# Kernel tuning notes

Measured on AMD Instinct MI355X. Metric: run time of the kernel, lower is better.

## Reference

```python
import jax, jax.numpy as jnp
import numpy as np

FACTOR = 5  # sampling factor c

def setup_inputs() -> dict:
    key = jax.random.key(0)
    k1, k2, k3, k4 = jax.random.split(key, 4)
    B, H, L, D = 4, 8, 2048, 64
    u = min(max(1, FACTOR * int(np.ceil(np.log(L)))), L)  # sample_k = 40
    return {
        "queries": jax.random.normal(k1, (B, H, L, D), jnp.float32),
        "keys": jax.random.normal(k2, (B, H, L, D), jnp.float32),
        "values": jax.random.normal(k3, (B, H, L, D), jnp.float32),
        "index_sample": jax.random.randint(k4, (L, u), 0, L, jnp.int32),
    }

def reference(queries, keys, values, index_sample):
    B, H, L_Q, D = queries.shape
    L_K = keys.shape[2]
    scale = 1.0 / np.sqrt(D)
    U_part = min(max(1, FACTOR * int(np.ceil(np.log(L_K)))), L_Q)  # n_top queries

    # --- _prob_QK: sampled scores + sparsity measure ---
    # K_sample[b,h,q,s,:] = keys[b,h,index_sample[q,s],:]  -> (B,H,L_Q,u,D)
    K_sample = keys[:, :, index_sample, :]
    QK_sample = jnp.einsum('bhqd,bhqsd->bhqs', queries, K_sample)  # (B,H,L_Q,u)
    M = QK_sample.max(-1) - QK_sample.sum(-1) / L_K                # (B,H,L_Q)
    _, index = jax.lax.top_k(M, U_part)                            # (B,H,U)

    # --- initial context: mean of V for non-selected queries ---
    context = jnp.broadcast_to(values.mean(-2, keepdims=True), (B, H, L_Q, D))

    # --- full attention for the top-U queries only ---
    Q_reduce = jnp.take_along_axis(queries, index[..., None], axis=2)   # (B,H,U,D)
    scores = jnp.einsum('bhud,bhkd->bhuk', Q_reduce, keys) * scale      # (B,H,U,L_K)
    attn = jax.nn.softmax(scores, axis=-1)
    out = jnp.einsum('bhuk,bhkd->bhud', attn, values)                   # (B,H,U,D)

    # --- scatter selected outputs back into the mean context ---
    bi = jnp.arange(B)[:, None, None]
    hi = jnp.arange(H)[None, :, None]
    context = context.at[bi, hi, index].set(out)
    return context
```

## Files before the change

### kernel.cpp

```cpp
#include <hip/hip_runtime.h>
#include <math.h>

#define Bq 4
#define Hh 8
#define Lh 2048
#define Dh 64
#define BH (Bq*Hh)

__global__ __launch_bounds__(256) void kAC(const float* __restrict__ Q,
                                           const float* __restrict__ K,
                                           const float* __restrict__ V,
                                           const int* __restrict__ idxs,
                                           float2* __restrict__ M2,
                                           float* __restrict__ vpart, int u) {
    int bi = blockIdx.x;
    int tid = threadIdx.x;
    if (bi < 2048) {
        int xcd = bi & 7, slot = bi >> 3;
        int bh  = xcd * 4 + (slot >> 6);
        int qt  = (slot >> 1) & 31;
        int half = slot & 1;
        int wave = tid >> 6, lane = tid & 63;
        int g = lane >> 2, c = lane & 3;
        int q = qt * 64 + wave * 16 + g;
        long gq = (long)bh * Lh + q;

        const float* qrow = Q + gq * Dh;
        float4 qf[4];
#pragma unroll
        for (int jj = 0; jj < 4; ++jj)
            qf[jj] = *(const float4*)(qrow + jj * 16 + c * 4);

        int cnt1 = u >> 1;
        int c0 = (half == 0) ? (u - cnt1) : cnt1;
        const int* irow = idxs + (long)q * u + (half ? (u - cnt1) : 0);
        const float* kbase = K + (long)bh * Lh * Dh;

        float mx = -INFINITY, sm = 0.f;
        int s = 0;
        for (; s + 4 <= c0; s += 4) {
            int i0 = irow[s], i1 = irow[s+1], i2 = irow[s+2], i3 = irow[s+3];
            const float* kp0 = kbase + (long)i0 * Dh + c * 4;
            const float* kp1 = kbase + (long)i1 * Dh + c * 4;
            const float* kp2 = kbase + (long)i2 * Dh + c * 4;
            const float* kp3 = kbase + (long)i3 * Dh + c * 4;
            float4 kf[4][4];
#pragma unroll
            for (int jj = 0; jj < 4; ++jj) {
                kf[0][jj] = *(const float4*)(kp0 + jj * 16);
                kf[1][jj] = *(const float4*)(kp1 + jj * 16);
                kf[2][jj] = *(const float4*)(kp2 + jj * 16);
                kf[3][jj] = *(const float4*)(kp3 + jj * 16);
            }
            float a[4];
#pragma unroll
            for (int r = 0; r < 4; ++r) {
                float ac = 0.f;
#pragma unroll
                for (int jj = 0; jj < 4; ++jj)
                    ac += qf[jj].x*kf[r][jj].x + qf[jj].y*kf[r][jj].y
                        + qf[jj].z*kf[r][jj].z + qf[jj].w*kf[r][jj].w;
                a[r] = ac;
            }
#pragma unroll
            for (int r = 0; r < 4; ++r) {
                a[r] += __shfl_xor(a[r], 1);
                a[r] += __shfl_xor(a[r], 2);
                mx = fmaxf(mx, a[r]); sm += a[r];
            }
        }
        for (; s < c0; ++s) {
            int ki = irow[s];
            const float* krow = kbase + (long)ki * Dh + c * 4;
            float acc = 0.f;
#pragma unroll
            for (int jj = 0; jj < 4; ++jj) {
                float4 kf = *(const float4*)(krow + jj * 16);
                acc += qf[jj].x*kf.x + qf[jj].y*kf.y + qf[jj].z*kf.z + qf[jj].w*kf.w;
            }
            acc += __shfl_xor(acc, 1);
            acc += __shfl_xor(acc, 2);
            mx = fmaxf(mx, acc); sm += acc;
        }
        if (c == 0) M2[gq * 2 + half] = make_float2(mx, sm);
    } else {
        int b2 = bi - 2048;
        int xcd = b2 & 7, slot = b2 >> 3;
        int bh = xcd * 4 + (slot >> 3);
        int chunk = slot & 7;
        int d = tid & 63, r0 = tid >> 6;
        const float* vb = V + ((long)bh * Lh + chunk * 256) * Dh;
        float s = 0.f;
        for (int i = 0; i < 64; ++i) s += vb[(r0 + 4 * i) * Dh + d];
        __shared__ float part[4][64];
        part[r0][d] = s;
        __syncthreads();
        if (tid < 64) {
            float t = part[0][tid] + part[1][tid] + part[2][tid] + part[3][tid];
            vpart[(bh * 8 + chunk) * 64 + tid] = t;
        }
    }
}

__global__ __launch_bounds__(256) void kBE(const float2* __restrict__ M2,
                                           const float* __restrict__ vpart,
                                           int* __restrict__ topk,
                                           float* __restrict__ ctx, int U) {
    int bi = blockIdx.x;
    int tid = threadIdx.x;
    if (bi < 4096) {
        long base = (long)bi * 1024;
        int bh = (int)(base >> 17);
        __shared__ float vm[64];
        if (tid < 64) {
            float s = 0.f;
#pragma unroll
            for (int c2 = 0; c2 < 8; ++c2) s += vpart[(bh * 8 + c2) * 64 + tid];
            vm[tid] = s * (1.0f / (float)Lh);
        }
        __syncthreads();
        float4 val = *(const float4*)(vm + ((tid * 4) & 63));
        *(float4*)(ctx + base + tid * 4) = val;
        return;
    }
    int bh = bi - 4096;
    unsigned key[8];
#pragma unroll
    for (int j = 0; j < 8; ++j) {
        long q = (long)bh * Lh + tid + 256 * j;
        float4 mm = *(const float4*)(&M2[q * 2]);
        float Mv = fmaxf(mm.x, mm.z) - (mm.y + mm.w) * (1.0f / (float)Lh);
        unsigned ub = __float_as_uint(Mv);
        key[j] = ub ^ ((ub >> 31) ? 0xFFFFFFFFu : 0x80000000u);
    }
    __shared__ unsigned hist[256];
    __shared__ unsigned prefix_s;
    __shared__ int need_s;
    if (tid == 0) { prefix_s = 0u; need_s = U; }

    for (int level = 3; level >= 0; --level) {
        int shift = level * 8;
        hist[tid] = 0u;
        __syncthreads();
        unsigned prefix = prefix_s;
        int need = need_s;
        unsigned pmask = (level == 3) ? 0u : (0xFFFFFFFFu << (shift + 8));
#pragma unroll
        for (int j = 0; j < 8; ++j)
            if ((key[j] & pmask) == prefix)
                atomicAdd(&hist[(key[j] >> shift) & 0xFF], 1u);
        __syncthreads();
        if (tid < 64) {
            int lane = tid;
            unsigned h0 = hist[lane*4+0], h1 = hist[lane*4+1],
                     h2 = hist[lane*4+2], h3 = hist[lane*4+3];
            unsigned lt = h0 + h1 + h2 + h3;
            unsigned ssum = lt;
#pragma unroll
            for (int off = 1; off < 64; off <<= 1) {
                unsigned t = __shfl_down(ssum, off);
                if (lane + off < 64) ssum += t;
            }
            unsigned sx  = ssum - lt;
            unsigned suf3 = sx  + h3;
            unsigned suf2 = suf3 + h2;
            unsigned suf1 = suf2 + h1;
            unsigned suf0 = suf1 + h0;
            int localb = -1; unsigned nxt = 0u;
            if      ((int)suf3 >= need) { localb = lane*4+3; nxt = sx;   }
            else if ((int)suf2 >= need) { localb = lane*4+2; nxt = suf3; }
            else if ((int)suf1 >= need) { localb = lane*4+1; nxt = suf2; }
            else if ((int)suf0 >= need) { localb = lane*4+0; nxt = suf1; }
            unsigned long long ball = __ballot(localb >= 0);
            int hilane = 63 - __clzll(ball);
            if (lane == hilane) {
                prefix_s = prefix | ((unsigned)localb << shift);
                need_s = need - (int)nxt;
            }
        }
        __syncthreads();
    }
    unsigned T = prefix_s;
    int r = need_s;
    __shared__ int cgt, ceq;
    if (tid == 0) { cgt = 0; ceq = 0; }
    __syncthreads();
    int* out = topk + bh * U;
#pragma unroll
    for (int j = 0; j < 8; ++j) {
        if (key[j] > T) { int p = atomicAdd(&cgt, 1); out[p] = tid + 256 * j; }
        else if (key[j] == T) { int e = atomicAdd(&ceq, 1); if (e < r) out[U - r + e] = tid + 256 * j; }
    }
}

#define TK 64
__global__ __launch_bounds__(256) void kD_part(const float* __restrict__ Q,
                                               const float* __restrict__ K,
                                               const float* __restrict__ V,
                                               const int* __restrict__ topk,
                                               float* __restrict__ pm,
                                               float* __restrict__ pl,
                                               float* __restrict__ pacc,
                                               int U, int nch) {
    int bi = blockIdx.x;
    int xcd = bi & 7, slot = bi >> 3;
    int per = nch * 8;
    int bh = xcd * 4 + slot / per;
    int rest = slot % per;
    int uc = rest >> 3, kc = rest & 7;

    int tid = threadIdx.x;
    int wv = tid >> 6, lane = tid & 63;

    __shared__ float Qs[8 * 64];
    __shared__ float Ks[TK * 68];
    __shared__ float Ps[8 * 68];
    __shared__ float alph[8], mst[8], lst[8];
    __shared__ int   qidxs[8];
    float* accbuf = Ks;

    if (tid < 8) {
        int gu = uc * 8 + tid;
        qidxs[tid] = (gu < U) ? topk[bh * U + gu] : 0;
    }
    __syncthreads();
#pragma unroll
    for (int step = 0; step < 2; ++step) {
        int uu = step * 4 + wv;
        int row = qidxs[uu];
        Qs[uu * 64 + lane] = Q[((long)bh * Lh + row) * Dh + lane] * 0.125f;
    }

    int kq = lane, ug = wv;
    float mrun0 = -INFINITY, mrun1 = -INFINITY;
    float lrun0 = 0.f, lrun1 = 0.f;
    float accv[8] = {0.f,0.f,0.f,0.f,0.f,0.f,0.f,0.f};

    const long kvbase = (long)bh * Lh * Dh;
    const float4* Kg4 = (const float4*)(K + kvbase);
    const float*  Vg  = V + kvbase;
    int kbase0 = kc * 256;

    for (int t = 0; t < 4; ++t) {
        int t0 = kbase0 + t * TK;
        int f40 = t0 * (Dh / 4);
#pragma unroll
        for (int j = 0; j < 4; ++j) {
            int i = tid + 256 * j;
            float4 kv = Kg4[f40 + i];
            int row = i >> 4, col = i & 15;
            *(float4*)(&Ks[row * 68 + col * 4]) = kv;
        }
        __syncthreads();

        float s0 = 0.f, s1 = 0.f;
#pragma unroll
        for (int j16 = 0; j16 < 16; ++j16) {
            float4 kf = *(const float4*)(&Ks[kq * 68 + j16 * 4]);
            float4 qa = *(const float4*)(&Qs[(2 * ug + 0) * 64 + j16 * 4]);
            float4 qb = *(const float4*)(&Qs[(2 * ug + 1) * 64 + j16 * 4]);
            s0 += kf.x * qa.x + kf.y * qa.y + kf.z * qa.z + kf.w * qa.w;
            s1 += kf.x * qb.x + kf.y * qb.y + kf.z * qb.z + kf.w * qb.w;
        }
        float m0 = s0, m1 = s1;
#pragma unroll
        for (int off = 1; off < 64; off <<= 1) {
            m0 = fmaxf(m0, __shfl_xor(m0, off));
            m1 = fmaxf(m1, __shfl_xor(m1, off));
        }
        float mn0 = fmaxf(mrun0, m0), mn1 = fmaxf(mrun1, m1);
        float a0 = __expf(mrun0 - mn0), a1 = __expf(mrun1 - mn1);
        float p0 = __expf(s0 - mn0),  p1 = __expf(s1 - mn1);
        float ls0 = p0, ls1 = p1;
#pragma unroll
        for (int off = 1; off < 64; off <<= 1) {
            ls0 += __shfl_xor(ls0, off);
            ls1 += __shfl_xor(ls1, off);
        }
        lrun0 = a0 * lrun0 + ls0;  lrun1 = a1 * lrun1 + ls1;
        mrun0 = mn0;               mrun1 = mn1;
        Ps[(2 * ug + 0) * 68 + kq] = p0;
        Ps[(2 * ug + 1) * 68 + kq] = p1;
        if (lane == 0) { alph[2 * ug] = a0; alph[2 * ug + 1] = a1; }
        __syncthreads();

        float vk[16];
        int vrow0 = t0 + wv * 16;
#pragma unroll
        for (int k = 0; k < 16; ++k)
            vk[k] = Vg[(long)(vrow0 + k) * Dh + lane];
#pragma unroll
        for (int u2 = 0; u2 < 8; ++u2) {
            const float* pb = &Ps[u2 * 68 + wv * 16];
            float4 pA = *(const float4*)(pb + 0);
            float4 pB = *(const float4*)(pb + 4);
            float4 pC = *(const float4*)(pb + 8);
            float4 pD = *(const float4*)(pb + 12);
            float av = alph[u2];
            float ac = accv[u2] * av;
            ac += pA.x*vk[0]  + pA.y*vk[1]  + pA.z*vk[2]  + pA.w*vk[3];
            ac += pB.x*vk[4]  + pB.y*vk[5]  + pB.z*vk[6]  + pB.w*vk[7];
            ac += pC.x*vk[8]  + pC.y*vk[9]  + pC.z*vk[10] + pC.w*vk[11];
            ac += pD.x*vk[12] + pD.y*vk[13] + pD.z*vk[14] + pD.w*vk[15];
            accv[u2] = ac;
        }
    }

    if (lane == 0) {
        mst[2 * ug] = mrun0;     lst[2 * ug] = lrun0;
        mst[2 * ug + 1] = mrun1; lst[2 * ug + 1] = lrun1;
    }
#pragma unroll
    for (int u2 = 0; u2 < 8; ++u2)
        accbuf[wv * 512 + u2 * 64 + lane] = accv[u2];
    __syncthreads();

    int pbase = (bh * nch + uc) * 8;
    {
        int d = tid & 63, ua = tid >> 6;
#pragma unroll
        for (int h = 0; h < 2; ++h) {
            int u2 = ua + 4 * h;
            float o = accbuf[0 * 512 + u2 * 64 + d] + accbuf[1 * 512 + u2 * 64 + d]
                    + accbuf[2 * 512 + u2 * 64 + d] + accbuf[3 * 512 + u2 * 64 + d];
            pacc[((long)(pbase + u2) * 8 + kc) * 64 + d] = o;
        }
    }
    if (tid < 8) {
        int qp = (pbase + tid) * 8 + kc;
        pm[qp] = mst[tid];
        pl[qp] = lst[tid];
    }
}

__global__ __launch_bounds__(256) void kF_comb(const float* __restrict__ pm,
                                               const float* __restrict__ pl,
                                               const float* __restrict__ pacc,
                                               const int* __restrict__ topk,
                                               float* __restrict__ ctx,
                                               int U, int nch) {
    int bi = blockIdx.x;
    int bh = bi / nch, uc = bi % nch;
    int tid = threadIdx.x;
    int u = tid >> 5, t = tid & 31;
    int gu = uc * 8 + u;
    if (gu >= U) return;
    int qbase = (bh * nch + uc) * 8 + u;
    float m[8], l[8];
#pragma unroll
    for (int kc = 0; kc < 8; ++kc) { m[kc] = pm[qbase * 8 + kc]; l[kc] = pl[qbase * 8 + kc]; }
    float gm = m[0];
#pragma unroll
    for (int kc = 1; kc < 8; ++kc) gm = fmaxf(gm, m[kc]);
    float w[8]; float gl = 0.f;
#pragma unroll
    for (int kc = 0; kc < 8; ++kc) { w[kc] = __expf(m[kc] - gm); gl += l[kc] * w[kc]; }
    float inv = 1.0f / gl;
    float o0 = 0.f, o1 = 0.f;
#pragma unroll
    for (int kc = 0; kc < 8; ++kc) {
        const float* a = pacc + ((long)qbase * 8 + kc) * 64;
        o0 += a[t] * w[kc];
        o1 += a[t + 32] * w[kc];
    }
    int row = topk[bh * U + gu];
    float* crow = ctx + ((long)bh * Lh + row) * Dh;
    crow[t]      = o0 * inv;
    crow[t + 32] = o1 * inv;
}

extern "C" void kernel_launch(void* const* d_in, const int* in_sizes, int n_in,
                              void* d_out, int out_size, void* d_ws, size_t ws_size,
                              hipStream_t stream) {
    const float* Q    = (const float*)d_in[0];
    const float* K    = (const float*)d_in[1];
    const float* V    = (const float*)d_in[2];
    const int*   idxs = (const int*)d_in[3];
    float* ctx = (float*)d_out;

    int u = in_sizes[3] / Lh;
    int U = u;
    int nch = (U + 7) / 8;

    float*  wsf   = (float*)d_ws;
    float2* M2    = (float2*)wsf;
    int*    topk  = (int*)(wsf + 262144);
    float*  vpart = wsf + 262144 + 2048;
    float*  pm    = wsf + 280576;
    float*  pl    = pm + 32 * nch * 8 * 8;
    float*  pacc  = pl + 32 * nch * 8 * 8;

    kAC    <<<2304,         256, 0, stream>>>(Q, K, V, idxs, M2, vpart, u);
    kBE    <<<4128,         256, 0, stream>>>(M2, vpart, topk, ctx, U);
    kD_part<<<BH * nch * 8, 256, 0, stream>>>(Q, K, V, topk, pm, pl, pacc, U, nch);
    kF_comb<<<BH * nch,     256, 0, stream>>>(pm, pl, pacc, topk, ctx, U, nch);
}
```

Before: 154.4 us.

## Restructure sampled QK scoring: 16 lanes per query, full sample row per group

The sampled-score stage now gives each query to a 16-lane group, with one float4 of the 64-wide row per lane. Each group handles the whole sample list itself instead of splitting it into two halves, so M2 holds one (max,sum) pair per query and the top-k kernel no longer merges two partials. Sample indices are loaded once per 16 with a coalesced read and broadcast by shuffles. The V-mean blocks and the top-k blocks are moved to low block ids so they get scheduled first. In exchange the reductions need four shuffles per dot product, and each group has less independent work.

Result: slower. 159.9 us (+3.5%).

```diff
diff --git a/kernel.cpp b/kernel.cpp
--- a/kernel.cpp
+++ b/kernel.cpp
@@ -15,77 +15,74 @@
                                            float* __restrict__ vpart, int u) {
     int bi = blockIdx.x;
     int tid = threadIdx.x;
-    if (bi < 2048) {
+    if (bi >= 256) {
+        int b2 = bi - 256;
+        int xcd = b2 & 7, slot = b2 >> 3;
+        int bh  = xcd * 4 + (slot >> 6);
+        int q0  = (slot & 63) * 32;
+        int lane = tid & 63, wv = tid >> 6;
+        int g  = lane >> 4;
+        int j  = lane & 15;
+        int gb = lane & 48;
+        int grp = wv * 4 + g;
+
+        const float4* kb4 = (const float4*)(K + (long)bh * Lh * Dh);
+        const float4* qb4 = (const float4*)(Q + (long)bh * Lh * Dh);
+
+#define ROWS8(SOFF)                                                          \
+        {                                                                    \
+            float4 kf[8];                                                    \
+            _Pragma("unroll")                                                \
+            for (int r = 0; r < 8; ++r) {                                    \
+                int idx = __shfl(ireg, gb + (SOFF) + r);                     \
+                kf[r] = kb4[idx * 16 + j];                                   \
+            }                                                                \
+            _Pragma("unroll")                                                \
+            for (int r = 0; r < 8; ++r) {                                    \
+                float d = kf[r].x*qf.x + kf[r].y*qf.y                        \
+                        + kf[r].z*qf.z + kf[r].w*qf.w;                       \
+                d += __shfl_xor(d, 1);                                       \
+                d += __shfl_xor(d, 2);                                       \
+                d += __shfl_xor(d, 4);                                       \
+                d += __shfl_xor(d, 8);                                       \
+                mx = fmaxf(mx, d); sm += d;                                  \
+            }                                                                \
+        }
+
+#pragma unroll 1
+        for (int qq = 0; qq < 2; ++qq) {
+            int q = q0 + grp * 2 + qq;
+            float4 qf = qb4[q * 16 + j];
+            const int* irow = idxs + (long)q * u;
+            float mx = -INFINITY, sm = 0.f;
+
+            int base = 0;
+            int ireg = (j < u) ? irow[j] : 0;
+            while (base + 16 <= u) {
+                int iregN = (base + 16 + j < u) ? irow[base + 16 + j] : 0;
+                ROWS8(0)
+                ROWS8(8)
+                ireg = iregN;
+                base += 16;
+            }
+            int rem = u - base;
+            int s = 0;
+            if (rem >= 8) { ROWS8(0) s = 8; }
+            for (; s < rem; ++s) {
+                int idx = __shfl(ireg, gb + s);
+                float4 kf0 = kb4[idx * 16 + j];
+                float d = kf0.x*qf.x + kf0.y*qf.y + kf0.z*qf.z + kf0.w*qf.w;
+                d += __shfl_xor(d, 1);
+                d += __shfl_xor(d, 2);
+                d += __shfl_xor(d, 4);
+                d += __shfl_xor(d, 8);
+                mx = fmaxf(mx, d); sm += d;
+            }
+            if (j == 0) M2[(long)bh * Lh + q] = make_float2(mx, sm);
+        }
+#undef ROWS8
+    } else {
         int xcd = bi & 7, slot = bi >> 3;
-        int bh  = xcd * 4 + (slot >> 6);
-        int qt  = (slot >> 1) & 31;
-        int half = slot & 1;
-        int wave = tid >> 6, lane = tid & 63;
-        int g = lane >> 2, c = lane & 3;
-        int q = qt * 64 + wave * 16 + g;
-        long gq = (long)bh * Lh + q;
-
-        const float* qrow = Q + gq * Dh;
-        float4 qf[4];
-#pragma unroll
-        for (int jj = 0; jj < 4; ++jj)
-            qf[jj] = *(const float4*)(qrow + jj * 16 + c * 4);
-
-        int cnt1 = u >> 1;
-        int c0 = (half == 0) ? (u - cnt1) : cnt1;
-        const int* irow = idxs + (long)q * u + (half ? (u - cnt1) : 0);
-        const float* kbase = K + (long)bh * Lh * Dh;
-
-        float mx = -INFINITY, sm = 0.f;
-        int s = 0;
-        for (; s + 4 <= c0; s += 4) {
-            int i0 = irow[s], i1 = irow[s+1], i2 = irow[s+2], i3 = irow[s+3];
-            const float* kp0 = kbase + (long)i0 * Dh + c * 4;
-            const float* kp1 = kbase + (long)i1 * Dh + c * 4;
-            const float* kp2 = kbase + (long)i2 * Dh + c * 4;
-            const float* kp3 = kbase + (long)i3 * Dh + c * 4;
-            float4 kf[4][4];
-#pragma unroll
-            for (int jj = 0; jj < 4; ++jj) {
-                kf[0][jj] = *(const float4*)(kp0 + jj * 16);
-                kf[1][jj] = *(const float4*)(kp1 + jj * 16);
-                kf[2][jj] = *(const float4*)(kp2 + jj * 16);
-                kf[3][jj] = *(const float4*)(kp3 + jj * 16);
-            }
-            float a[4];
-#pragma unroll
-            for (int r = 0; r < 4; ++r) {
-                float ac = 0.f;
-#pragma unroll
-                for (int jj = 0; jj < 4; ++jj)
-                    ac += qf[jj].x*kf[r][jj].x + qf[jj].y*kf[r][jj].y
-                        + qf[jj].z*kf[r][jj].z + qf[jj].w*kf[r][jj].w;
-                a[r] = ac;
-            }
-#pragma unroll
-            for (int r = 0; r < 4; ++r) {
-                a[r] += __shfl_xor(a[r], 1);
-                a[r] += __shfl_xor(a[r], 2);
-                mx = fmaxf(mx, a[r]); sm += a[r];
-            }
-        }
-        for (; s < c0; ++s) {
-            int ki = irow[s];
-            const float* krow = kbase + (long)ki * Dh + c * 4;
-            float acc = 0.f;
-#pragma unroll
-            for (int jj = 0; jj < 4; ++jj) {
-                float4 kf = *(const float4*)(krow + jj * 16);
-                acc += qf[jj].x*kf.x + qf[jj].y*kf.y + qf[jj].z*kf.z + qf[jj].w*kf.w;
-            }
-            acc += __shfl_xor(acc, 1);
-            acc += __shfl_xor(acc, 2);
-            mx = fmaxf(mx, acc); sm += acc;
-        }
-        if (c == 0) M2[gq * 2 + half] = make_float2(mx, sm);
-    } else {
-        int b2 = bi - 2048;
-        int xcd = b2 & 7, slot = b2 >> 3;
         int bh = xcd * 4 + (slot >> 3);
         int chunk = slot & 7;
         int d = tid & 63, r0 = tid >> 6;
@@ -108,8 +105,8 @@
                                            float* __restrict__ ctx, int U) {
     int bi = blockIdx.x;
     int tid = threadIdx.x;
-    if (bi < 4096) {
-        long base = (long)bi * 1024;
+    if (bi >= 32) {
+        long base = (long)(bi - 32) * 1024;
         int bh = (int)(base >> 17);
         __shared__ float vm[64];
         if (tid < 64) {
@@ -123,13 +120,13 @@
         *(float4*)(ctx + base + tid * 4) = val;
         return;
     }
-    int bh = bi - 4096;
+    int bh = bi;
     unsigned key[8];
 #pragma unroll
     for (int j = 0; j < 8; ++j) {
         long q = (long)bh * Lh + tid + 256 * j;
-        float4 mm = *(const float4*)(&M2[q * 2]);
-        float Mv = fmaxf(mm.x, mm.z) - (mm.y + mm.w) * (1.0f / (float)Lh);
+        float2 mm = M2[q];
+        float Mv = mm.x - mm.y * (1.0f / (float)Lh);
         unsigned ub = __float_as_uint(Mv);
         key[j] = ub ^ ((ub >> 31) ? 0xFFFFFFFFu : 0x80000000u);
     }
@@ -384,9 +381,9 @@
 
     float*  wsf   = (float*)d_ws;
     float2* M2    = (float2*)wsf;
-    int*    topk  = (int*)(wsf + 262144);
-    float*  vpart = wsf + 262144 + 2048;
-    float*  pm    = wsf + 280576;
+    int*    topk  = (int*)(wsf + 131072);
+    float*  vpart = wsf + 131072 + 2048;
+    float*  pm    = wsf + 149504;
     float*  pl    = pm + 32 * nch * 8 * 8;
     float*  pacc  = pl + 32 * nch * 8 * 8;
 
```

## Double-buffer sampled K loads and reorder blocks so long-running work launches first

Applied to the files above, without the earlier changes.

The sampled-score loop now keeps two register buffers of four gathered K rows and issues the next group's loads before reducing the current group, so gather latency overlaps with the dot products. Block roles in both fused kernels are swapped so the V-mean and top-k blocks get the lowest block indices and are dispatched before the bulk work. A min-blocks hint of 2 is added to the launch bounds to cap register use. The doubled register buffers raise register pressure, and the reordering only helps if the host launch grids match the new index split.

New measurement: 236.0 us. +52.8%, slower.

```diff
diff --git a/kernel.cpp b/kernel.cpp
--- a/kernel.cpp
+++ b/kernel.cpp
@@ -7,16 +7,17 @@
 #define Dh 64
 #define BH (Bq*Hh)
 
-__global__ __launch_bounds__(256) void kAC(const float* __restrict__ Q,
-                                           const float* __restrict__ K,
-                                           const float* __restrict__ V,
-                                           const int* __restrict__ idxs,
-                                           float2* __restrict__ M2,
-                                           float* __restrict__ vpart, int u) {
+__global__ __launch_bounds__(256, 2) void kAC(const float* __restrict__ Q,
+                                              const float* __restrict__ K,
+                                              const float* __restrict__ V,
+                                              const int* __restrict__ idxs,
+                                              float2* __restrict__ M2,
+                                              float* __restrict__ vpart, int u) {
     int bi = blockIdx.x;
     int tid = threadIdx.x;
-    if (bi < 2048) {
-        int xcd = bi & 7, slot = bi >> 3;
+    if (bi >= 256) {
+        int b2 = bi - 256;
+        int xcd = b2 & 7, slot = b2 >> 3;
         int bh  = xcd * 4 + (slot >> 6);
         int qt  = (slot >> 1) & 31;
         int half = slot & 1;
@@ -38,36 +39,77 @@
 
         float mx = -INFINITY, sm = 0.f;
         int s = 0;
-        for (; s + 4 <= c0; s += 4) {
-            int i0 = irow[s], i1 = irow[s+1], i2 = irow[s+2], i3 = irow[s+3];
-            const float* kp0 = kbase + (long)i0 * Dh + c * 4;
-            const float* kp1 = kbase + (long)i1 * Dh + c * 4;
-            const float* kp2 = kbase + (long)i2 * Dh + c * 4;
-            const float* kp3 = kbase + (long)i3 * Dh + c * 4;
-            float4 kf[4][4];
-#pragma unroll
-            for (int jj = 0; jj < 4; ++jj) {
-                kf[0][jj] = *(const float4*)(kp0 + jj * 16);
-                kf[1][jj] = *(const float4*)(kp1 + jj * 16);
-                kf[2][jj] = *(const float4*)(kp2 + jj * 16);
-                kf[3][jj] = *(const float4*)(kp3 + jj * 16);
-            }
-            float a[4];
-#pragma unroll
-            for (int r = 0; r < 4; ++r) {
-                float ac = 0.f;
-#pragma unroll
-                for (int jj = 0; jj < 4; ++jj)
-                    ac += qf[jj].x*kf[r][jj].x + qf[jj].y*kf[r][jj].y
-                        + qf[jj].z*kf[r][jj].z + qf[jj].w*kf[r][jj].w;
-                a[r] = ac;
-            }
-#pragma unroll
-            for (int r = 0; r < 4; ++r) {
-                a[r] += __shfl_xor(a[r], 1);
-                a[r] += __shfl_xor(a[r], 2);
-                mx = fmaxf(mx, a[r]); sm += a[r];
-            }
+
+#define KLOAD(BUF, I0, I1, I2, I3)                                           \
+        {                                                                    \
+            const float* kp0 = kbase + (long)(I0) * Dh + c * 4;              \
+            const float* kp1 = kbase + (long)(I1) * Dh + c * 4;              \
+            const float* kp2 = kbase + (long)(I2) * Dh + c * 4;              \
+            const float* kp3 = kbase + (long)(I3) * Dh + c * 4;              \
+            _Pragma("unroll")                                                \
+            for (int jj = 0; jj < 4; ++jj) {                                 \
+                BUF[0][jj] = *(const float4*)(kp0 + jj * 16);                \
+                BUF[1][jj] = *(const float4*)(kp1 + jj * 16);                \
+                BUF[2][jj] = *(const float4*)(kp2 + jj * 16);                \
+                BUF[3][jj] = *(const float4*)(kp3 + jj * 16);                \
+            }                                                                \
+        }
+
+#define KCOMP(BUF)                                                           \
+        {                                                                    \
+            _Pragma("unroll")                                                \
+            for (int r = 0; r < 4; ++r) {                                    \
+                float a = 0.f;                                               \
+                _Pragma("unroll")                                            \
+                for (int jj = 0; jj < 4; ++jj)                               \
+                    a += qf[jj].x*BUF[r][jj].x + qf[jj].y*BUF[r][jj].y       \
+                       + qf[jj].z*BUF[r][jj].z + qf[jj].w*BUF[r][jj].w;      \
+                a += __shfl_xor(a, 1);                                       \
+                a += __shfl_xor(a, 2);                                       \
+                mx = fmaxf(mx, a); sm += a;                                  \
+            }                                                                \
+        }
+
+        if (c0 >= 8) {
+            float4 A[4][4], Bv[4][4];
+            {
+                int i0 = irow[0], i1 = irow[1], i2 = irow[2], i3 = irow[3];
+                KLOAD(A, i0, i1, i2, i3);
+            }
+            {
+                int i0 = irow[4], i1 = irow[5], i2 = irow[6], i3 = irow[7];
+                KLOAD(Bv, i0, i1, i2, i3);
+            }
+            s = 8;
+            while (s + 8 <= c0) {
+                int j0 = irow[s],     j1 = irow[s + 1],
+                    j2 = irow[s + 2], j3 = irow[s + 3];
+                int k0 = irow[s + 4], k1 = irow[s + 5],
+                    k2 = irow[s + 6], k3 = irow[s + 7];
+                KCOMP(A);
+                KLOAD(A, j0, j1, j2, j3);
+                KCOMP(Bv);
+                KLOAD(Bv, k0, k1, k2, k3);
+                s += 8;
+            }
+            if (s + 4 <= c0) {
+                int j0 = irow[s],     j1 = irow[s + 1],
+                    j2 = irow[s + 2], j3 = irow[s + 3];
+                KCOMP(A);
+                KLOAD(A, j0, j1, j2, j3);
+                s += 4;
+                KCOMP(Bv);
+                KCOMP(A);
+            } else {
+                KCOMP(A);
+                KCOMP(Bv);
+            }
+        } else if (c0 >= 4) {
+            float4 A[4][4];
+            int i0 = irow[0], i1 = irow[1], i2 = irow[2], i3 = irow[3];
+            KLOAD(A, i0, i1, i2, i3);
+            s = 4;
+            KCOMP(A);
         }
         for (; s < c0; ++s) {
             int ki = irow[s];
@@ -82,10 +124,11 @@
             acc += __shfl_xor(acc, 2);
             mx = fmaxf(mx, acc); sm += acc;
         }
+#undef KLOAD
+#undef KCOMP
         if (c == 0) M2[gq * 2 + half] = make_float2(mx, sm);
     } else {
-        int b2 = bi - 2048;
-        int xcd = b2 & 7, slot = b2 >> 3;
+        int xcd = bi & 7, slot = bi >> 3;
         int bh = xcd * 4 + (slot >> 3);
         int chunk = slot & 7;
         int d = tid & 63, r0 = tid >> 6;
@@ -108,8 +151,8 @@
                                            float* __restrict__ ctx, int U) {
     int bi = blockIdx.x;
     int tid = threadIdx.x;
-    if (bi < 4096) {
-        long base = (long)bi * 1024;
+    if (bi >= 32) {
+        long base = (long)(bi - 32) * 1024;
         int bh = (int)(base >> 17);
         __shared__ float vm[64];
         if (tid < 64) {
@@ -123,7 +166,7 @@
         *(float4*)(ctx + base + tid * 4) = val;
         return;
     }
-    int bh = bi - 4096;
+    int bh = bi;
     unsigned key[8];
 #pragma unroll
     for (int j = 0; j < 8; ++j) {
```
